# Performance work log

Measured on AMD Instinct MI355X. Metric: run time of the kernel, lower is better.

## Reference

```python
import jax, jax.numpy as jnp
import numpy as np

N_NODES = 50000
N_EDGES = 800000
N_GRAPHS = 32
D = 300
NUM_CLASSES = 40


def setup_inputs() -> dict:
    key = jax.random.key(0)
    ks = jax.random.split(key, 32)

    def w(k, shape):
        fan_in = shape[-2]
        return (jax.random.normal(k, shape, jnp.float32) / np.sqrt(fan_in)).astype(jnp.float32)

    inp = {
        'x': jax.random.normal(ks[0], (N_NODES, 3), jnp.float32),
        'edge_index': jax.random.randint(ks[1], (2, N_EDGES), 0, N_NODES, jnp.int32),
        'batch': jnp.sort(jax.random.randint(ks[2], (N_NODES,), 0, N_GRAPHS, jnp.int32)),
        # project MLP [3, 64, 128, 300]
        'pW1': w(ks[3], (3, 64)),   'pb1': jnp.zeros((64,), jnp.float32),
        'pW2': w(ks[4], (64, 128)), 'pb2': jnp.zeros((128,), jnp.float32),
        'pW3': w(ks[5], (128, D)),  'pb3': jnp.zeros((D,), jnp.float32),
        # 3 PointGNNConv layers, params stacked on leading axis
        'hW': w(ks[6], (3, D, 3)),      'hb': jnp.zeros((3, 3), jnp.float32),
        'fW': w(ks[7], (3, D + 3, D)),  'fb': jnp.zeros((3, D), jnp.float32),
        'gW': w(ks[8], (3, D, D)),      'gb': jnp.zeros((3, D), jnp.float32),
        # 3 post-conv linear layers [300, 300]
        'lW': w(ks[9], (3, D, D)),      'lb': jnp.zeros((3, D), jnp.float32),
        # decision head
        'dW': w(ks[10], (D, NUM_CLASSES)), 'db': jnp.zeros((NUM_CLASSES,), jnp.float32),
    }
    return inp


def reference(x, edge_index, batch, pW1, pb1, pW2, pb2, pW3, pb3,
              hW, hb, fW, fb, gW, gb, lW, lb, dW, db):
    pos = x  # [N, 3] raw point coordinates
    src, dst = edge_index[0], edge_index[1]  # j -> i (source_to_target)

    # embed MLP (eval mode: dropout/batchnorm are identity)
    h = jax.nn.relu(x @ pW1 + pb1)
    h = jax.nn.relu(h @ pW2 + pb2)
    h = h @ pW3 + pb3  # [N, 300]

    for i in range(3):
        # PointGNNConv: delta = mlp_h(x_i); e = mlp_f([pos_j - pos_i + delta_i, x_j]); max-aggr; mlp_g + residual
        delta = h @ hW[i] + hb[i]                     # [N, 3]
        rel = pos[src] - pos[dst] + delta[dst]        # [E, 3]
        e = jnp.concatenate([rel, h[src]], axis=1) @ fW[i] + fb[i]  # [E, 300]
        agg = jax.ops.segment_max(e, dst, num_segments=N_NODES)    # [N, 300]
        agg = jnp.where(jnp.isfinite(agg), agg, 0.0)  # zero-degree nodes -> 0
        h = agg @ gW[i] + gb[i] + h                   # residual
        h = jax.nn.relu(h)
        h = h @ lW[i] + lb[i]                         # lin_i

    # global mean pool over graphs
    sums = jax.ops.segment_sum(h, batch, num_segments=N_GRAPHS)           # [G, 300]
    cnt = jax.ops.segment_sum(jnp.ones((h.shape[0],), h.dtype), batch, num_segments=N_GRAPHS)
    mean = sums / jnp.maximum(cnt, 1.0)[:, None]

    logits = mean @ dW + db  # [G, 40]
    return jax.nn.log_softmax(logits, axis=1)
```

## Files before the change

kernel.cpp:

```cpp
#include <hip/hip_runtime.h>
#include <hip/hip_bf16.h>

#define DD 300
#define DP 320

typedef unsigned short ushort_t;
typedef __attribute__((ext_vector_type(8))) short short8;
typedef __attribute__((ext_vector_type(4))) float f32x4;

__device__ __forceinline__ float b2f(ushort_t u) {
    unsigned x = ((unsigned)u) << 16;
    return __uint_as_float(x);
}
__device__ __forceinline__ ushort_t f2b(float f) {
    unsigned u = __float_as_uint(f);
    unsigned r = (u + 0x7FFFu + ((u >> 16) & 1u)) >> 16;
    return (ushort_t)r;
}

__device__ __forceinline__ void gload16(const void* g, void* l) {
    __builtin_amdgcn_global_load_lds((const __attribute__((address_space(1))) void*)g,
                                     (__attribute__((address_space(3))) void*)l, 16, 0, 0);
}

template<int BNT, int BIAS, int RELU, int RESID, int RANK3>
__launch_bounds__(512)
__global__ void gemm_mfma(const ushort_t* __restrict__ A, int strideA, int M, int K,
                          const ushort_t* __restrict__ Bt,
                          const float* __restrict__ bias,
                          const ushort_t* __restrict__ resid,
                          const float* __restrict__ X3,
                          const float* __restrict__ W3,
                          int NCOL,
                          ushort_t* __restrict__ C, int strideC)
{
    constexpr int BM = 128, BK = 64, BN = 32 * BNT;
    constexpr int CA = BM * BK * 2 / 1024;
    constexpr int CB = BN * BK * 2 / 1024;
    constexpr int WCOLS = 16 * BNT;
    __shared__ ushort_t As[BM * BK];
    __shared__ ushort_t Bs[BN * BK];

    int bx = blockIdx.x, by = blockIdx.y;
    if (gridDim.x == 2 && (gridDim.y & 7) == 0) {
        int flat = bx + (by << 1);
        int xcd = flat & 7;
        int slot = flat >> 3;
        int rpx = gridDim.y >> 3;
        by = xcd * rpx + (slot >> 1);
        bx = slot & 1;
    }

    const int tid = threadIdx.x;
    const int lane = tid & 63, wid = tid >> 6;
    const int rowTile = by * BM;
    const int colTile = bx * BN;
    const int wm = wid >> 1, wn = wid & 1;

    const int lrow = lane >> 3;
    const int l8b = (lane & 7) * 16;

    f32x4 acc[2][BNT];
    #pragma unroll
    for (int f = 0; f < 2; ++f)
        #pragma unroll
        for (int q = 0; q < BNT; ++q) {
            f32x4 z = {0.f, 0.f, 0.f, 0.f};
            acc[f][q] = z;
        }

    for (int k0 = 0; k0 < K; k0 += BK) {
        for (int c = wid; c < CA; c += 8) {
            int row = c * 8 + lrow;
            int colb = l8b ^ ((row & 7) << 4);
            int gr = rowTile + row; if (gr > M - 1) gr = M - 1;
            gload16(A + (size_t)gr * strideA + k0 + (colb >> 1), As + c * 512);
        }
        for (int c = wid; c < CB; c += 8) {
            int row = c * 8 + lrow;
            int colb = l8b ^ ((row & 7) << 4);
            gload16(Bt + (size_t)(colTile + row) * K + k0 + (colb >> 1), Bs + c * 512);
        }
        __syncthreads();

        #pragma unroll
        for (int ks = 0; ks < 2; ++ks) {
            const int kidx = ks * 32 + (lane >> 4) * 8;
            short8 af[2], bf[BNT];
            #pragma unroll
            for (int f = 0; f < 2; ++f) {
                int row = wm * 32 + f * 16 + (lane & 15);
                int phys = (row * 128 + kidx * 2) ^ ((row & 7) << 4);
                af[f] = *(const short8*)((const char*)As + phys);
            }
            #pragma unroll
            for (int q = 0; q < BNT; ++q) {
                int row = wn * WCOLS + q * 16 + (lane & 15);
                int phys = (row * 128 + kidx * 2) ^ ((row & 7) << 4);
                bf[q] = *(const short8*)((const char*)Bs + phys);
            }
            #pragma unroll
            for (int f = 0; f < 2; ++f)
                #pragma unroll
                for (int q = 0; q < BNT; ++q)
                    acc[f][q] = __builtin_amdgcn_mfma_f32_16x16x32_bf16(af[f], bf[q], acc[f][q], 0, 0, 0);
        }
        __syncthreads();
    }

    ushort_t* eb = Bs + wid * 16 * WCOLS;
    #pragma unroll
    for (int f = 0; f < 2; ++f) {
        #pragma unroll
        for (int q = 0; q < BNT; ++q) {
            #pragma unroll
            for (int r = 0; r < 4; ++r) {
                int rl = (lane >> 4) * 4 + r;
                int row = rowTile + wm * 32 + f * 16 + rl;
                int rr = row < M ? row : M - 1;
                int col = colTile + wn * WCOLS + q * 16 + (lane & 15);
                float v = acc[f][q][r];
                if (BIAS) v += bias[col];
                if (RANK3) {
                    if (col < NCOL) {
                        v += X3[rr * 3 + 0] * W3[col]
                           + X3[rr * 3 + 1] * W3[NCOL + col]
                           + X3[rr * 3 + 2] * W3[2 * NCOL + col];
                    }
                }
                if (RESID) v += b2f(resid[(size_t)rr * strideC + col]);
                if (RELU) v = fmaxf(v, 0.f);
                eb[rl * WCOLS + q * 16 + (lane & 15)] = f2b(v);
            }
        }
        for (int ch = lane; ch < 32 * BNT; ch += 64) {
            int rl = ch / (2 * BNT);
            int cc = ch - rl * (2 * BNT);
            int row = rowTile + wm * 32 + f * 16 + rl;
            if (row < M) {
                short8 vv = *(const short8*)(eb + rl * WCOLS + cc * 8);
                *(short8*)(C + (size_t)row * strideC + colTile + wn * WCOLS + cc * 8) = vv;
            }
        }
    }
}

__global__ void prep(const float* __restrict__ pW2, const float* __restrict__ pW3,
                     const float* __restrict__ pb3,
                     const float* __restrict__ hW, const float* __restrict__ hb,
                     const float* __restrict__ fW,
                     const float* __restrict__ gW, const float* __restrict__ gb,
                     const float* __restrict__ lW, const float* __restrict__ lb,
                     ushort_t* __restrict__ WU, ushort_t* __restrict__ WG,
                     ushort_t* __restrict__ WL, ushort_t* __restrict__ W2,
                     ushort_t* __restrict__ W3e,
                     float* __restrict__ bU, float* __restrict__ bG,
                     float* __restrict__ bL, float* __restrict__ b3)
{
    const int SZ = DP * DP;
    int idx = blockIdx.x * 256 + threadIdx.x;
    if (idx < 3 * SZ) {
        int i = idx / SZ, r = idx - i * SZ;
        int n = r / DP, k = r - n * DP;
        float v = 0.f;
        if (k < DD) {
            if (n < DD) v = fW[i * 90900 + (3 + k) * DD + n];
            else if (n < DD + 3) v = hW[i * 900 + k * 3 + (n - DD)];
        }
        WU[idx] = f2b(v);
        return;
    }
    idx -= 3 * SZ;
    if (idx < 3 * SZ) {
        int i = idx / SZ, r = idx - i * SZ;
        int n = r / DP, k = r - n * DP;
        float v = (n < DD && k < DD) ? gW[i * 90000 + k * DD + n] : 0.f;
        WG[idx] = f2b(v);
        return;
    }
    idx -= 3 * SZ;
    if (idx < 3 * SZ) {
        int i = idx / SZ, r = idx - i * SZ;
        int n = r / DP, k = r - n * DP;
        float v = (n < DD && k < DD) ? lW[i * 90000 + k * DD + n] : 0.f;
        WL[idx] = f2b(v);
        return;
    }
    idx -= 3 * SZ;
    if (idx < 128 * 64) {
        int n = idx >> 6, k = idx & 63;
        W2[idx] = f2b(pW2[k * 128 + n]);
        return;
    }
    idx -= 128 * 64;
    if (idx < DP * 128) {
        int n = idx >> 7, k = idx & 127;
        W3e[idx] = f2b((n < DD) ? pW3[k * DD + n] : 0.f);
        return;
    }
    idx -= DP * 128;
    if (idx < 3 * DP) {
        int i = idx / DP, n = idx - i * DP;
        bU[idx] = (n >= DD && n < DD + 3) ? hb[i * 3 + (n - DD)] : 0.f;
        return;
    }
    idx -= 3 * DP;
    if (idx < 3 * DP) {
        int i = idx / DP, n = idx - i * DP;
        bG[idx] = (n < DD) ? gb[i * DD + n] : 0.f;
        return;
    }
    idx -= 3 * DP;
    if (idx < 3 * DP) {
        int i = idx / DP, n = idx - i * DP;
        bL[idx] = (n < DD) ? lb[i * DD + n] : 0.f;
        return;
    }
    idx -= 3 * DP;
    if (idx < DP) {
        b3[idx] = (idx < DD) ? pb3[idx] : 0.f;
        return;
    }
}

__global__ void embed1(const float* __restrict__ x, const float* __restrict__ W,
                       const float* __restrict__ b, ushort_t* __restrict__ h1, int M)
{
    int idx = blockIdx.x * 256 + threadIdx.x;
    if (idx >= M * 64) return;
    int n = idx >> 6, c = idx & 63;
    const float* xr = x + n * 3;
    float v = xr[0] * W[c] + xr[1] * W[64 + c] + xr[2] * W[128 + c] + b[c];
    h1[idx] = f2b(fmaxf(v, 0.f));
}

__global__ void hist_kernel(const int* __restrict__ dst, int* __restrict__ cnt, int E)
{
    int e = blockIdx.x * 256 + threadIdx.x;
    if (e < E) atomicAdd(&cnt[dst[e]], 1);
}
__global__ void scan1(const int* __restrict__ cnt, int* __restrict__ bsum, int N)
{
    __shared__ int s[256];
    int t = threadIdx.x;
    int i = blockIdx.x * 256 + t;
    s[t] = (i < N) ? cnt[i] : 0;
    __syncthreads();
    for (int o = 128; o > 0; o >>= 1) { if (t < o) s[t] += s[t + o]; __syncthreads(); }
    if (t == 0) bsum[blockIdx.x] = s[0];
}
__global__ void scan2(int* __restrict__ bsum, int nb)
{
    __shared__ int s[256];
    int t = threadIdx.x;
    int v = (t < nb) ? bsum[t] : 0;
    s[t] = v; __syncthreads();
    for (int o = 1; o < 256; o <<= 1) {
        int x = (t >= o) ? s[t - o] : 0;
        __syncthreads();
        s[t] += x;
        __syncthreads();
    }
    if (t < nb) bsum[t] = s[t] - v;
}
__global__ void scan3(const int* __restrict__ cnt, const int* __restrict__ bsumx,
                      int* __restrict__ off, int* __restrict__ cursor, int N)
{
    __shared__ int s[256];
    int t = threadIdx.x;
    int i = blockIdx.x * 256 + t;
    int v = (i < N) ? cnt[i] : 0;
    s[t] = v; __syncthreads();
    for (int o = 1; o < 256; o <<= 1) {
        int x = (t >= o) ? s[t - o] : 0;
        __syncthreads();
        s[t] += x;
        __syncthreads();
    }
    int excl = s[t] - v + bsumx[blockIdx.x];
    if (i <= N) {
        off[i] = excl;
        if (i < N) cursor[i] = excl;
    }
}
__global__ void scatter_kernel(const int* __restrict__ src, const int* __restrict__ dst,
                               int* __restrict__ cursor, int* __restrict__ csr, int E)
{
    int e = blockIdx.x * 256 + threadIdx.x;
    if (e < E) {
        int p = atomicAdd(&cursor[dst[e]], 1);
        csr[p] = src[e];
    }
}

__global__ void segmax(const ushort_t* __restrict__ u, const int* __restrict__ off,
                       const int* __restrict__ csr,
                       const float* __restrict__ x, const float* __restrict__ fWp,
                       const float* __restrict__ fb, ushort_t* __restrict__ agg, int Nn)
{
    int n = blockIdx.x * 4 + (threadIdx.x >> 6);
    int lane = threadIdx.x & 63;
    if (n >= Nn) return;
    const int e0 = off[n], e1 = off[n + 1];

    const ushort_t* un = u + (size_t)n * DP;
    float d0 = b2f(un[300]) - x[n * 3 + 0];
    float d1 = b2f(un[301]) - x[n * 3 + 1];
    float d2 = b2f(un[302]) - x[n * 3 + 2];

    float m[5];
    #pragma unroll
    for (int j = 0; j < 5; ++j) m[j] = -INFINITY;

    int e = e0;
    for (; e + 3 < e1; e += 4) {
        const ushort_t* r0 = u + (size_t)csr[e]     * DP + lane;
        const ushort_t* r1 = u + (size_t)csr[e + 1] * DP + lane;
        const ushort_t* r2 = u + (size_t)csr[e + 2] * DP + lane;
        const ushort_t* r3 = u + (size_t)csr[e + 3] * DP + lane;
        #pragma unroll
        for (int j = 0; j < 5; ++j) {
            float a = fmaxf(b2f(r0[64 * j]), b2f(r1[64 * j]));
            float b = fmaxf(b2f(r2[64 * j]), b2f(r3[64 * j]));
            m[j] = fmaxf(m[j], fmaxf(a, b));
        }
    }
    for (; e < e1; ++e) {
        const ushort_t* r0 = u + (size_t)csr[e] * DP + lane;
        #pragma unroll
        for (int j = 0; j < 5; ++j) m[j] = fmaxf(m[j], b2f(r0[64 * j]));
    }

    #pragma unroll
    for (int j = 0; j < 5; ++j) {
        int col = lane + 64 * j;
        float o = 0.f;
        if (e1 > e0 && col < DD)
            o = m[j] + fb[col] + d0 * fWp[col] + d1 * fWp[DD + col] + d2 * fWp[2 * DD + col];
        agg[(size_t)n * DP + col] = f2b(o);
    }
}

__global__ void pool_kernel(const ushort_t* __restrict__ h, const int* __restrict__ batch,
                            float* __restrict__ sums, float* __restrict__ cnts,
                            int Nn, int npb)
{
    int c = threadIdx.x;
    int n0 = blockIdx.x * npb;
    int n1 = min(n0 + npb, Nn);
    if (n0 >= n1) return;
    if (c < DD) {
        float run = 0.f;
        int g = batch[n0];
        for (int n = n0; n < n1; ++n) {
            int gn = batch[n];
            if (gn != g) { atomicAdd(&sums[g * DD + c], run); run = 0.f; g = gn; }
            run += b2f(h[(size_t)n * DP + c]);
        }
        atomicAdd(&sums[g * DD + c], run);
    } else if (c == DD) {
        float run = 0.f;
        int g = batch[n0];
        for (int n = n0; n < n1; ++n) {
            int gn = batch[n];
            if (gn != g) { atomicAdd(&cnts[g], run); run = 0.f; g = gn; }
            run += 1.f;
        }
        atomicAdd(&cnts[g], run);
    }
}

__global__ void head_kernel(const float* __restrict__ sums, const float* __restrict__ cnts,
                            const float* __restrict__ dW, const float* __restrict__ db,
                            float* __restrict__ out)
{
    __shared__ float mean[32][DD];
    __shared__ float logits[32][40];
    int tid = threadIdx.x;
    for (int i = tid; i < 32 * DD; i += 256) {
        int g = i / DD;
        mean[g][i - g * DD] = sums[i] / fmaxf(cnts[g], 1.f);
    }
    __syncthreads();
    for (int o = tid; o < 32 * 40; o += 256) {
        int g = o / 40, cls = o - g * 40;
        float acc = db[cls];
        for (int k = 0; k < DD; ++k) acc += mean[g][k] * dW[k * 40 + cls];
        logits[g][cls] = acc;
    }
    __syncthreads();
    if (tid < 32) {
        float mx = -INFINITY;
        #pragma unroll
        for (int j = 0; j < 40; ++j) mx = fmaxf(mx, logits[tid][j]);
        float se = 0.f;
        for (int j = 0; j < 40; ++j) se += expf(logits[tid][j] - mx);
        float lse = mx + logf(se);
        for (int j = 0; j < 40; ++j) out[tid * 40 + j] = logits[tid][j] - lse;
    }
}

extern "C" void kernel_launch(void* const* d_in, const int* in_sizes, int n_in,
                              void* d_out, int out_size, void* d_ws, size_t ws_size,
                              hipStream_t stream)
{
    const float* x     = (const float*)d_in[0];
    const int*   ei    = (const int*)d_in[1];
    const int*   batch = (const int*)d_in[2];
    const float* pW1   = (const float*)d_in[3];
    const float* pb1   = (const float*)d_in[4];
    const float* pW2   = (const float*)d_in[5];
    const float* pb2   = (const float*)d_in[6];
    const float* pW3   = (const float*)d_in[7];
    const float* pb3   = (const float*)d_in[8];
    const float* hW    = (const float*)d_in[9];
    const float* hb    = (const float*)d_in[10];
    const float* fW    = (const float*)d_in[11];
    const float* fb    = (const float*)d_in[12];
    const float* gW    = (const float*)d_in[13];
    const float* gb    = (const float*)d_in[14];
    const float* lW    = (const float*)d_in[15];
    const float* lb    = (const float*)d_in[16];
    const float* dW    = (const float*)d_in[17];
    const float* db    = (const float*)d_in[18];

    const int N = in_sizes[0] / 3;
    const int E = in_sizes[1] / 2;
    const int G = 32;
    const int SZ = DP * DP;
    (void)ws_size; (void)n_in; (void)out_size;

    char* wsb = (char*)d_ws;
    size_t offb = 0;
    auto alloc = [&](size_t bytes) {
        void* p = wsb + offb;
        offb += (bytes + 255) & ~(size_t)255;
        return p;
    };
    ushort_t* h    = (ushort_t*)alloc((size_t)N * DP * 2);
    ushort_t* u    = (ushort_t*)alloc((size_t)N * DP * 2);
    ushort_t* agg  = (ushort_t*)alloc((size_t)N * DP * 2);
    ushort_t* h1   = (ushort_t*)alloc((size_t)N * 64 * 2);
    ushort_t* h2   = (ushort_t*)alloc((size_t)N * 128 * 2);
    ushort_t* WU   = (ushort_t*)alloc((size_t)3 * SZ * 2);
    ushort_t* WG   = (ushort_t*)alloc((size_t)3 * SZ * 2);
    ushort_t* WL   = (ushort_t*)alloc((size_t)3 * SZ * 2);
    ushort_t* W2   = (ushort_t*)alloc((size_t)128 * 64 * 2);
    ushort_t* W3e  = (ushort_t*)alloc((size_t)DP * 128 * 2);
    float*    bU   = (float*)alloc((size_t)3 * DP * 4);
    float*    bG   = (float*)alloc((size_t)3 * DP * 4);
    float*    bL   = (float*)alloc((size_t)3 * DP * 4);
    float*    b3   = (float*)alloc((size_t)DP * 4);
    int*      cnt    = (int*)alloc((size_t)(N + 1) * 4);
    int*      offp   = (int*)alloc((size_t)(N + 1) * 4);
    int*      cursor = (int*)alloc((size_t)N * 4);
    int*      bsum   = (int*)alloc((size_t)256 * 4);
    int*      csr    = (int*)alloc((size_t)E * 4);
    float*    sums   = (float*)alloc((size_t)(G * DD + G) * 4);
    float*    cnts   = sums + G * DD;

    const int* srcp = ei;
    const int* dstp = ei + E;
    const int nb = (N + 255) / 256;
    const dim3 blk(256);
    const int rowBlocks = (N + 127) / 128;
    const int rowBlocksPad = ((rowBlocks + 7) / 8) * 8;

    const int prepTotal = 3 * SZ * 3 + 128 * 64 + DP * 128 + 3 * DP * 3 + DP;
    prep<<<dim3((prepTotal + 255) / 256), blk, 0, stream>>>(
        pW2, pW3, pb3, hW, hb, fW, gW, gb, lW, lb,
        WU, WG, WL, W2, W3e, bU, bG, bL, b3);

    hipMemsetAsync(cnt, 0, (size_t)(N + 1) * 4, stream);
    hist_kernel<<<dim3((E + 255) / 256), blk, 0, stream>>>(dstp, cnt, E);
    scan1<<<dim3(nb), blk, 0, stream>>>(cnt, bsum, N);
    scan2<<<dim3(1), blk, 0, stream>>>(bsum, nb);
    scan3<<<dim3(nb), blk, 0, stream>>>(cnt, bsum, offp, cursor, N);
    scatter_kernel<<<dim3((E + 255) / 256), blk, 0, stream>>>(srcp, dstp, cursor, csr, E);

    embed1<<<dim3((N * 64 + 255) / 256), blk, 0, stream>>>(x, pW1, pb1, h1, N);
    gemm_mfma<4, 1, 1, 0, 0><<<dim3(1, rowBlocks), dim3(512), 0, stream>>>(
        h1, 64, N, 64, W2, pb2, nullptr, nullptr, nullptr, 128, h2, 128);
    gemm_mfma<5, 1, 0, 0, 0><<<dim3(2, rowBlocksPad), dim3(512), 0, stream>>>(
        h2, 128, N, 128, W3e, b3, nullptr, nullptr, nullptr, DD, h, DP);

    for (int i = 0; i < 3; ++i) {
        const float* fWi = fW + (size_t)i * 90900;
        const float* fbi = fb + (size_t)i * DD;

        gemm_mfma<5, 1, 0, 0, 1><<<dim3(2, rowBlocksPad), dim3(512), 0, stream>>>(
            h, DP, N, DP, WU + (size_t)i * SZ, bU + (size_t)i * DP,
            nullptr, x, fWi, DD, u, DP);

        segmax<<<dim3((N + 3) / 4), blk, 0, stream>>>(u, offp, csr, x, fWi, fbi, agg, N);

        gemm_mfma<5, 1, 1, 1, 0><<<dim3(2, rowBlocksPad), dim3(512), 0, stream>>>(
            agg, DP, N, DP, WG + (size_t)i * SZ, bG + (size_t)i * DP,
            h, nullptr, nullptr, DD, u, DP);

        gemm_mfma<5, 1, 0, 0, 0><<<dim3(2, rowBlocksPad), dim3(512), 0, stream>>>(
            u, DP, N, DP, WL + (size_t)i * SZ, bL + (size_t)i * DP,
            nullptr, nullptr, nullptr, DD, h, DP);
    }

    hipMemsetAsync(sums, 0, (size_t)(G * DD + G) * 4, stream);
    pool_kernel<<<dim3((N + 127) / 128), dim3(320), 0, stream>>>(h, batch, sums, cnts, N, 128);
    head_kernel<<<dim3(1), dim3(256), 0, stream>>>(sums, cnts, dW, db, (float*)d_out);
}
```

Measured before the change: 686.3 us.

## Split segment-max across column slices and precompute per-node delta offsets

The max-aggregation kernel now launches eight blocks per group of four nodes. Each block's waves cover one 40-column slice of the 320-wide bf16 row instead of all five 64-column chunks. A small new kernel computes the per-node position delta into a float4 buffer, so the segmax epilogue no longer reads it from the wide row. The aim is more waves in flight for the latency-bound gather. The cost is that only 40 of 64 lanes do useful work, the CSR indices are re-read eight times, and there is an extra kernel launch per layer.

```diff
diff --git a/kernel.cpp b/kernel.cpp
--- a/kernel.cpp
+++ b/kernel.cpp
@@ -3,6 +3,7 @@
 
 #define DD 300
 #define DP 320
+#define SLW 40
 
 typedef unsigned short ushort_t;
 typedef __attribute__((ext_vector_type(8))) short short8;
@@ -293,50 +294,58 @@
     }
 }
 
+__global__ void dltext(const ushort_t* __restrict__ u, const float* __restrict__ x,
+                       float4* __restrict__ dlt, int Nn)
+{
+    int n = blockIdx.x * 256 + threadIdx.x;
+    if (n >= Nn) return;
+    const ushort_t* un = u + (size_t)n * DP;
+    float4 d;
+    d.x = b2f(un[300]) - x[n * 3 + 0];
+    d.y = b2f(un[301]) - x[n * 3 + 1];
+    d.z = b2f(un[302]) - x[n * 3 + 2];
+    d.w = 0.f;
+    dlt[n] = d;
+}
+
 __global__ void segmax(const ushort_t* __restrict__ u, const int* __restrict__ off,
-                       const int* __restrict__ csr,
-                       const float* __restrict__ x, const float* __restrict__ fWp,
-                       const float* __restrict__ fb, ushort_t* __restrict__ agg, int Nn)
-{
-    int n = blockIdx.x * 4 + (threadIdx.x >> 6);
+                       const int* __restrict__ csr, const float4* __restrict__ dlt,
+                       const float* __restrict__ fWp, const float* __restrict__ fb,
+                       ushort_t* __restrict__ agg, int Nn)
+{
+    int bid = blockIdx.x;
+    int slice = bid & 7;
+    int n = (bid >> 3) * 4 + (threadIdx.x >> 6);
     int lane = threadIdx.x & 63;
     if (n >= Nn) return;
     const int e0 = off[n], e1 = off[n + 1];
-
-    const ushort_t* un = u + (size_t)n * DP;
-    float d0 = b2f(un[300]) - x[n * 3 + 0];
-    float d1 = b2f(un[301]) - x[n * 3 + 1];
-    float d2 = b2f(un[302]) - x[n * 3 + 2];
-
-    float m[5];
-    #pragma unroll
-    for (int j = 0; j < 5; ++j) m[j] = -INFINITY;
-
+    const int colBase = slice * SLW;
+    const int cl = lane < SLW ? lane : SLW - 1;
+    const ushort_t* ub = u + colBase + cl;
+
+    float m = -INFINITY;
     int e = e0;
     for (; e + 3 < e1; e += 4) {
-        const ushort_t* r0 = u + (size_t)csr[e]     * DP + lane;
-        const ushort_t* r1 = u + (size_t)csr[e + 1] * DP + lane;
-        const ushort_t* r2 = u + (size_t)csr[e + 2] * DP + lane;
-        const ushort_t* r3 = u + (size_t)csr[e + 3] * DP + lane;
-        #pragma unroll
-        for (int j = 0; j < 5; ++j) {
-            float a = fmaxf(b2f(r0[64 * j]), b2f(r1[64 * j]));
-            float b = fmaxf(b2f(r2[64 * j]), b2f(r3[64 * j]));
-            m[j] = fmaxf(m[j], fmaxf(a, b));
-        }
+        int s0 = __builtin_nontemporal_load(csr + e);
+        int s1 = __builtin_nontemporal_load(csr + e + 1);
+        int s2 = __builtin_nontemporal_load(csr + e + 2);
+        int s3 = __builtin_nontemporal_load(csr + e + 3);
+        float a = fmaxf(b2f(ub[(size_t)s0 * DP]), b2f(ub[(size_t)s1 * DP]));
+        float b = fmaxf(b2f(ub[(size_t)s2 * DP]), b2f(ub[(size_t)s3 * DP]));
+        m = fmaxf(m, fmaxf(a, b));
     }
     for (; e < e1; ++e) {
-        const ushort_t* r0 = u + (size_t)csr[e] * DP + lane;
-        #pragma unroll
-        for (int j = 0; j < 5; ++j) m[j] = fmaxf(m[j], b2f(r0[64 * j]));
-    }
-
-    #pragma unroll
-    for (int j = 0; j < 5; ++j) {
-        int col = lane + 64 * j;
+        int s0 = __builtin_nontemporal_load(csr + e);
+        m = fmaxf(m, b2f(ub[(size_t)s0 * DP]));
+    }
+
+    if (lane < SLW) {
+        int col = colBase + lane;
         float o = 0.f;
-        if (e1 > e0 && col < DD)
-            o = m[j] + fb[col] + d0 * fWp[col] + d1 * fWp[DD + col] + d2 * fWp[2 * DD + col];
+        if (e1 > e0 && col < DD) {
+            float4 d = dlt[n];
+            o = m + fb[col] + d.x * fWp[col] + d.y * fWp[DD + col] + d.z * fWp[2 * DD + col];
+        }
         agg[(size_t)n * DP + col] = f2b(o);
     }
 }
@@ -442,6 +451,7 @@
     ushort_t* agg  = (ushort_t*)alloc((size_t)N * DP * 2);
     ushort_t* h1   = (ushort_t*)alloc((size_t)N * 64 * 2);
     ushort_t* h2   = (ushort_t*)alloc((size_t)N * 128 * 2);
+    float4*   dlt4 = (float4*)alloc((size_t)N * 16);
     ushort_t* WU   = (ushort_t*)alloc((size_t)3 * SZ * 2);
     ushort_t* WG   = (ushort_t*)alloc((size_t)3 * SZ * 2);
     ushort_t* WL   = (ushort_t*)alloc((size_t)3 * SZ * 2);
@@ -492,7 +502,10 @@
             h, DP, N, DP, WU + (size_t)i * SZ, bU + (size_t)i * DP,
             nullptr, x, fWi, DD, u, DP);
 
-        segmax<<<dim3((N + 3) / 4), blk, 0, stream>>>(u, offp, csr, x, fWi, fbi, agg, N);
+        dltext<<<dim3((N + 255) / 256), blk, 0, stream>>>(u, x, dlt4, N);
+
+        segmax<<<dim3(8 * ((N + 3) / 4)), blk, 0, stream>>>(
+            u, offp, csr, dlt4, fWi, fbi, agg, N);
 
         gemm_mfma<5, 1, 1, 1, 0><<<dim3(2, rowBlocksPad), dim3(512), 0, stream>>>(
             agg, DP, N, DP, WG + (size_t)i * SZ, bG + (size_t)i * DP,
```

Result: slower. 1.433 ms (+108.8%).
